# Optimization experiments

Measured on AMD Instinct MI355X. Metric: run time of the kernel, lower is better.

Reference implementation:

```python
import jax, jax.numpy as jnp
import numpy as np

EPS = 1e-5


def setup_inputs() -> dict:
    key = jax.random.key(0)
    ks = jax.random.split(key, 5)
    B, C, H, W = 64, 512, 28, 28
    G = 8
    c_half = C // (2 * G)  # 32
    return {
        "x": jax.random.normal(ks[0], (B, C, H, W), dtype=jnp.float32),
        "cweight": jax.random.normal(ks[1], (c_half,), dtype=jnp.float32),
        "cbias": jax.random.normal(ks[2], (c_half,), dtype=jnp.float32),
        "sweight": jax.random.normal(ks[3], (c_half,), dtype=jnp.float32),
        "sbias": jax.random.normal(ks[4], (c_half,), dtype=jnp.float32),
        "G": G,
    }


def reference(x, cweight, cbias, sweight, sbias, G):
    B, C, H, W = x.shape
    HW = H * W
    Cg = C // G
    c_half = Cg // 2

    # group view: [B*G, Cg, HW]
    xg = x.reshape(B * G, Cg, HW)
    x0 = xg[:, :c_half]   # channel-attention half
    x1 = xg[:, c_half:]   # spatial-attention half

    # channel attention: sigmoid(cweight * avgpool_hw(x0) + cbias), per channel
    m = jnp.mean(x0, axis=-1, keepdims=True)                    # [BG, c_half, 1]
    a0 = jax.nn.sigmoid(cweight[None, :, None] * m + cbias[None, :, None])
    y0 = x0 * a0

    # spatial attention: GN stats over the whole c_half*HW slab per (b,g)
    mu = jnp.mean(x1, axis=(1, 2), keepdims=True)               # [BG, 1, 1]
    var = jnp.mean(x1 * x1, axis=(1, 2), keepdims=True) - mu * mu
    rstd = jax.lax.rsqrt(jnp.maximum(var, 0.0) + EPS)
    norm = (x1 - mu) * rstd
    a1 = jax.nn.sigmoid(sweight[None, :, None] * norm + sbias[None, :, None])
    y1 = x1 * a1

    y = jnp.concatenate([y0, y1], axis=1).reshape(B, C, HW)

    # channel shuffle with 2 groups: out[:, 2*w + g2] = y[:, g2*(C//2) + w]
    y = y.reshape(B, 2, C // 2, HW).transpose(0, 2, 1, 3).reshape(B, C, H, W)
    return y
```

## Files before the change

### kernel.cpp

```cpp
#include <hip/hip_runtime.h>

typedef float f32x4 __attribute__((ext_vector_type(4)));

#define EPSV 1e-5f

__device__ __forceinline__ float sigmoidf_(float z) {
    return 1.0f / (1.0f + __expf(-z));
}

__global__ __launch_bounds__(1024, 4) void fused_sgate_onepass(
    const f32x4* __restrict__ x4,
    const float* __restrict__ cweight,
    const float* __restrict__ cbias,
    const float* __restrict__ sweight,
    const float* __restrict__ sbias,
    f32x4* __restrict__ out4,
    int nX1)
{
    const int tid = threadIdx.x;

    if ((int)blockIdx.x < nX1) {
        const int bg = blockIdx.x;
        const int b  = bg >> 3, g = bg & 7;
        const f32x4* __restrict__ xs = x4 + (size_t)bg * 12544 + 6272;

        f32x4 w[6];
#pragma unroll
        for (int k = 0; k < 6; ++k) w[k] = xs[tid + 1024 * k];
        const bool x1e = (tid < 128);
        f32x4 we = {0.f, 0.f, 0.f, 0.f};
        if (x1e) we = xs[6144 + tid];

        float s = 0.f, ss = 0.f;
#pragma unroll
        for (int k = 0; k < 6; ++k) {
            s  += (w[k].x + w[k].y) + (w[k].z + w[k].w);
            ss += (w[k].x * w[k].x + w[k].y * w[k].y)
                + (w[k].z * w[k].z + w[k].w * w[k].w);
        }
        s  += (we.x + we.y) + (we.z + we.w);
        ss += (we.x * we.x + we.y * we.y) + (we.z * we.z + we.w * we.w);

#pragma unroll
        for (int m = 32; m >= 1; m >>= 1) {
            s  += __shfl_xor(s,  m, 64);
            ss += __shfl_xor(ss, m, 64);
        }

        __shared__ float lds_s[16], lds_ss[16];
        __shared__ float ldsA[32], ldsB[32];
        if ((tid & 63) == 0) { lds_s[tid >> 6] = s; lds_ss[tid >> 6] = ss; }
        __syncthreads();

        if (tid < 32) {
            float S = 0.f, SS = 0.f;
#pragma unroll
            for (int i = 0; i < 16; ++i) { S += lds_s[i]; SS += lds_ss[i]; }
            constexpr float inv_n = 1.0f / (32.0f * 784.0f);
            const float mu   = S * inv_n;
            const float var  = SS * inv_n - mu * mu;
            const float rstd = rsqrtf(fmaxf(var, 0.f) + EPSV);
            const float A    = sweight[tid] * rstd;
            ldsA[tid] = A;
            ldsB[tid] = sbias[tid] - A * mu;
        }
        __syncthreads();

#pragma unroll
        for (int k = 0; k < 6; ++k)
            asm volatile("" : "+v"(w[k].x), "+v"(w[k].y),
                              "+v"(w[k].z), "+v"(w[k].w));

        f32x4* __restrict__ ob = out4 + (size_t)b * 100352;
#pragma unroll
        for (int k = 0; k < 6; ++k) {
            const int idx = tid + 1024 * k;
            const int c1  = idx / 196;
            const int p   = idx - c1 * 196;
            const float A = ldsA[c1], Bq = ldsB[c1];
            f32x4 t = w[k], r;
            r.x = t.x * sigmoidf_(A * t.x + Bq);
            r.y = t.y * sigmoidf_(A * t.y + Bq);
            r.z = t.z * sigmoidf_(A * t.z + Bq);
            r.w = t.w * sigmoidf_(A * t.w + Bq);
            const int c  = g * 64 + 32 + c1;
            const int cp = (c < 256) ? (2 * c) : (2 * (c - 256) + 1);
            __builtin_nontemporal_store(r, ob + (size_t)cp * 196 + p);
        }
        if (x1e) {
            const int idx = 6144 + tid;
            const int c1  = idx / 196;
            const int p   = idx - c1 * 196;
            const float A = ldsA[c1], Bq = ldsB[c1];
            f32x4 t = we, r;
            r.x = t.x * sigmoidf_(A * t.x + Bq);
            r.y = t.y * sigmoidf_(A * t.y + Bq);
            r.z = t.z * sigmoidf_(A * t.z + Bq);
            r.w = t.w * sigmoidf_(A * t.w + Bq);
            const int c  = g * 64 + 32 + c1;
            const int cp = (c < 256) ? (2 * c) : (2 * (c - 256) + 1);
            __builtin_nontemporal_store(r, ob + (size_t)cp * 196 + p);
        }
    } else {
        const int chw = ((int)blockIdx.x - nX1) * 16 + (tid >> 6);
        const int ln  = tid & 63;
        const int bg  = chw >> 5;
        const int cc  = chw & 31;

        const f32x4* __restrict__ xch = x4 + (size_t)bg * 12544 + cc * 196;
        f32x4 v0 = xch[ln];
        f32x4 v1 = xch[64 + ln];
        f32x4 v2 = xch[128 + ln];
        const bool extra = (ln < 4);
        f32x4 v3 = {0.f, 0.f, 0.f, 0.f};
        if (extra) v3 = xch[192 + ln];

        float s = (v0.x + v0.y) + (v0.z + v0.w)
                + (v1.x + v1.y) + (v1.z + v1.w)
                + (v2.x + v2.y) + (v2.z + v2.w)
                + (v3.x + v3.y) + (v3.z + v3.w);
#pragma unroll
        for (int m = 32; m >= 1; m >>= 1) s += __shfl_xor(s, m, 64);

        const float a0 = sigmoidf_(cweight[cc] * (s * (1.0f / 784.0f)) + cbias[cc]);

        const int b = bg >> 3, g = bg & 7;
        const int c  = g * 64 + cc;
        const int cp = (c < 256) ? (2 * c) : (2 * (c - 256) + 1);
        f32x4* __restrict__ och = out4 + (size_t)b * 100352 + (size_t)cp * 196;

        __builtin_nontemporal_store(v0 * a0, &och[ln]);
        __builtin_nontemporal_store(v1 * a0, &och[64 + ln]);
        __builtin_nontemporal_store(v2 * a0, &och[128 + ln]);
        if (extra) __builtin_nontemporal_store(v3 * a0, &och[192 + ln]);
    }
}

extern "C" void kernel_launch(void* const* d_in, const int* in_sizes, int n_in,
                              void* d_out, int out_size, void* d_ws, size_t ws_size,
                              hipStream_t stream) {
    const float* x  = (const float*)d_in[0];
    const float* cw = (const float*)d_in[1];
    const float* cb = (const float*)d_in[2];
    const float* sw = (const float*)d_in[3];
    const float* sb = (const float*)d_in[4];
    float* out = (float*)d_out;

    const int B   = in_sizes[0] / (512 * 784);
    const int nX1 = B * 8;
    const int nX0 = B * 16;

    fused_sgate_onepass<<<nX1 + nX0, 1024, 0, stream>>>(
        (const f32x4*)x, cw, cb, sw, sb, (f32x4*)out, nX1);
}
```

Baseline: 193.9 us.

## Interleave spatial and channel blocks, halve block size, reload x1 slab instead of caching

```diff
diff --git a/kernel.cpp b/kernel.cpp
--- a/kernel.cpp
+++ b/kernel.cpp
@@ -8,38 +8,35 @@
     return 1.0f / (1.0f + __expf(-z));
 }
 
-__global__ __launch_bounds__(1024, 4) void fused_sgate_onepass(
+__global__ __launch_bounds__(512, 8) void fused_sgate_mix(
     const f32x4* __restrict__ x4,
     const float* __restrict__ cweight,
     const float* __restrict__ cbias,
     const float* __restrict__ sweight,
     const float* __restrict__ sbias,
-    f32x4* __restrict__ out4,
-    int nX1)
+    f32x4* __restrict__ out4)
 {
+    const int bid = (int)blockIdx.x;
     const int tid = threadIdx.x;
 
-    if ((int)blockIdx.x < nX1) {
-        const int bg = blockIdx.x;
+    if (bid % 5 == 0) {
+        const int bg = bid / 5;
         const int b  = bg >> 3, g = bg & 7;
         const f32x4* __restrict__ xs = x4 + (size_t)bg * 12544 + 6272;
 
-        f32x4 w[6];
-#pragma unroll
-        for (int k = 0; k < 6; ++k) w[k] = xs[tid + 1024 * k];
-        const bool x1e = (tid < 128);
-        f32x4 we = {0.f, 0.f, 0.f, 0.f};
-        if (x1e) we = xs[6144 + tid];
-
         float s = 0.f, ss = 0.f;
 #pragma unroll
-        for (int k = 0; k < 6; ++k) {
-            s  += (w[k].x + w[k].y) + (w[k].z + w[k].w);
-            ss += (w[k].x * w[k].x + w[k].y * w[k].y)
-                + (w[k].z * w[k].z + w[k].w * w[k].w);
+        for (int k = 0; k < 12; ++k) {
+            f32x4 v = xs[tid + 512 * k];
+            s  += (v.x + v.y) + (v.z + v.w);
+            ss += (v.x * v.x + v.y * v.y) + (v.z * v.z + v.w * v.w);
         }
-        s  += (we.x + we.y) + (we.z + we.w);
-        ss += (we.x * we.x + we.y * we.y) + (we.z * we.z + we.w * we.w);
+        const bool x1e = (tid < 128);
+        if (x1e) {
+            f32x4 v = xs[6144 + tid];
+            s  += (v.x + v.y) + (v.z + v.w);
+            ss += (v.x * v.x + v.y * v.y) + (v.z * v.z + v.w * v.w);
+        }
 
 #pragma unroll
         for (int m = 32; m >= 1; m >>= 1) {
@@ -47,7 +44,7 @@
             ss += __shfl_xor(ss, m, 64);
         }
 
-        __shared__ float lds_s[16], lds_ss[16];
+        __shared__ float lds_s[8], lds_ss[8];
         __shared__ float ldsA[32], ldsB[32];
         if ((tid & 63) == 0) { lds_s[tid >> 6] = s; lds_ss[tid >> 6] = ss; }
         __syncthreads();
@@ -55,7 +52,7 @@
         if (tid < 32) {
             float S = 0.f, SS = 0.f;
 #pragma unroll
-            for (int i = 0; i < 16; ++i) { S += lds_s[i]; SS += lds_ss[i]; }
+            for (int i = 0; i < 8; ++i) { S += lds_s[i]; SS += lds_ss[i]; }
             constexpr float inv_n = 1.0f / (32.0f * 784.0f);
             const float mu   = S * inv_n;
             const float var  = SS * inv_n - mu * mu;
@@ -66,19 +63,14 @@
         }
         __syncthreads();
 
-#pragma unroll
-        for (int k = 0; k < 6; ++k)
-            asm volatile("" : "+v"(w[k].x), "+v"(w[k].y),
-                              "+v"(w[k].z), "+v"(w[k].w));
-
         f32x4* __restrict__ ob = out4 + (size_t)b * 100352;
 #pragma unroll
-        for (int k = 0; k < 6; ++k) {
-            const int idx = tid + 1024 * k;
+        for (int k = 0; k < 12; ++k) {
+            const int idx = tid + 512 * k;
             const int c1  = idx / 196;
             const int p   = idx - c1 * 196;
             const float A = ldsA[c1], Bq = ldsB[c1];
-            f32x4 t = w[k], r;
+            f32x4 t = xs[idx], r;
             r.x = t.x * sigmoidf_(A * t.x + Bq);
             r.y = t.y * sigmoidf_(A * t.y + Bq);
             r.z = t.z * sigmoidf_(A * t.z + Bq);
@@ -92,7 +84,7 @@
             const int c1  = idx / 196;
             const int p   = idx - c1 * 196;
             const float A = ldsA[c1], Bq = ldsB[c1];
-            f32x4 t = we, r;
+            f32x4 t = xs[idx], r;
             r.x = t.x * sigmoidf_(A * t.x + Bq);
             r.y = t.y * sigmoidf_(A * t.y + Bq);
             r.z = t.z * sigmoidf_(A * t.z + Bq);
@@ -102,10 +94,11 @@
             __builtin_nontemporal_store(r, ob + (size_t)cp * 196 + p);
         }
     } else {
-        const int chw = ((int)blockIdx.x - nX1) * 16 + (tid >> 6);
-        const int ln  = tid & 63;
-        const int bg  = chw >> 5;
-        const int cc  = chw & 31;
+        const int x0id = bid - bid / 5 - 1;
+        const int chw  = x0id * 8 + (tid >> 6);
+        const int ln   = tid & 63;
+        const int bg   = chw >> 5;
+        const int cc   = chw & 31;
 
         const f32x4* __restrict__ xch = x4 + (size_t)bg * 12544 + cc * 196;
         f32x4 v0 = xch[ln];
@@ -148,8 +141,8 @@
 
     const int B   = in_sizes[0] / (512 * 784);
     const int nX1 = B * 8;
-    const int nX0 = B * 16;
+    const int nX0 = B * 32;
 
-    fused_sgate_onepass<<<nX1 + nX0, 1024, 0, stream>>>(
-        (const f32x4*)x, cw, cb, sw, sb, (f32x4*)out, nX1);
+    fused_sgate_mix<<<nX1 + nX0, 512, 0, stream>>>(
+        (const f32x4*)x, cw, cb, sw, sb, (f32x4*)out);
 }
```

Result: slower. 219.5 us (+13.2%).

## Stage spatial-half slab in LDS to cut registers and double occupancy

Applied to the files above, without the earlier changes.

```diff
diff --git a/kernel.cpp b/kernel.cpp
--- a/kernel.cpp
+++ b/kernel.cpp
@@ -8,7 +8,7 @@
     return 1.0f / (1.0f + __expf(-z));
 }
 
-__global__ __launch_bounds__(1024, 4) void fused_sgate_onepass(
+__global__ __launch_bounds__(1024, 8) void fused_sgate_lds(
     const f32x4* __restrict__ x4,
     const float* __restrict__ cweight,
     const float* __restrict__ cbias,
@@ -24,31 +24,40 @@
         const int b  = bg >> 3, g = bg & 7;
         const f32x4* __restrict__ xs = x4 + (size_t)bg * 12544 + 6272;
 
-        f32x4 w[6];
-#pragma unroll
-        for (int k = 0; k < 6; ++k) w[k] = xs[tid + 1024 * k];
+        __shared__ f32x4 slab[4096];
+        __shared__ float lds_s[16], lds_ss[16];
+        __shared__ float ldsA[32], ldsB[32];
+
+        f32x4 t0 = xs[tid];
+        f32x4 t1 = xs[1024 + tid];
+        f32x4 t2 = xs[2048 + tid];
+        f32x4 t3 = xs[3072 + tid];
+        f32x4 w0 = xs[4096 + tid];
+        f32x4 w1 = xs[5120 + tid];
         const bool x1e = (tid < 128);
         f32x4 we = {0.f, 0.f, 0.f, 0.f};
         if (x1e) we = xs[6144 + tid];
 
-        float s = 0.f, ss = 0.f;
-#pragma unroll
-        for (int k = 0; k < 6; ++k) {
-            s  += (w[k].x + w[k].y) + (w[k].z + w[k].w);
-            ss += (w[k].x * w[k].x + w[k].y * w[k].y)
-                + (w[k].z * w[k].z + w[k].w * w[k].w);
+        slab[tid]        = t0;
+        slab[1024 + tid] = t1;
+        slab[2048 + tid] = t2;
+        slab[3072 + tid] = t3;
+
+        float s, ss;
+        {
+            f32x4 a = t0 + t1, c = t2 + t3, d = w0 + w1;
+            f32x4 q = t0 * t0 + t1 * t1 + t2 * t2 + t3 * t3
+                    + w0 * w0 + w1 * w1 + we * we;
+            f32x4 sv = a + c + d + we;
+            s  = (sv.x + sv.y) + (sv.z + sv.w);
+            ss = (q.x + q.y) + (q.z + q.w);
         }
-        s  += (we.x + we.y) + (we.z + we.w);
-        ss += (we.x * we.x + we.y * we.y) + (we.z * we.z + we.w * we.w);
 
 #pragma unroll
         for (int m = 32; m >= 1; m >>= 1) {
             s  += __shfl_xor(s,  m, 64);
             ss += __shfl_xor(ss, m, 64);
         }
-
-        __shared__ float lds_s[16], lds_ss[16];
-        __shared__ float ldsA[32], ldsB[32];
         if ((tid & 63) == 0) { lds_s[tid >> 6] = s; lds_ss[tid >> 6] = ss; }
         __syncthreads();
 
@@ -66,40 +75,66 @@
         }
         __syncthreads();
 
-#pragma unroll
-        for (int k = 0; k < 6; ++k)
-            asm volatile("" : "+v"(w[k].x), "+v"(w[k].y),
-                              "+v"(w[k].z), "+v"(w[k].w));
+        asm volatile("" : "+v"(w0.x), "+v"(w0.y), "+v"(w0.z), "+v"(w0.w),
+                          "+v"(w1.x), "+v"(w1.y), "+v"(w1.z), "+v"(w1.w));
 
         f32x4* __restrict__ ob = out4 + (size_t)b * 100352;
 #pragma unroll
-        for (int k = 0; k < 6; ++k) {
+        for (int k = 0; k < 4; ++k) {
             const int idx = tid + 1024 * k;
             const int c1  = idx / 196;
             const int p   = idx - c1 * 196;
             const float A = ldsA[c1], Bq = ldsB[c1];
-            f32x4 t = w[k], r;
-            r.x = t.x * sigmoidf_(A * t.x + Bq);
-            r.y = t.y * sigmoidf_(A * t.y + Bq);
-            r.z = t.z * sigmoidf_(A * t.z + Bq);
-            r.w = t.w * sigmoidf_(A * t.w + Bq);
+            f32x4 v = slab[idx], r;
+            r.x = v.x * sigmoidf_(A * v.x + Bq);
+            r.y = v.y * sigmoidf_(A * v.y + Bq);
+            r.z = v.z * sigmoidf_(A * v.z + Bq);
+            r.w = v.w * sigmoidf_(A * v.w + Bq);
             const int c  = g * 64 + 32 + c1;
             const int cp = (c < 256) ? (2 * c) : (2 * (c - 256) + 1);
-            __builtin_nontemporal_store(r, ob + (size_t)cp * 196 + p);
+            ob[(size_t)cp * 196 + p] = r;
+        }
+        {
+            const int idx = 4096 + tid;
+            const int c1  = idx / 196;
+            const int p   = idx - c1 * 196;
+            const float A = ldsA[c1], Bq = ldsB[c1];
+            f32x4 r;
+            r.x = w0.x * sigmoidf_(A * w0.x + Bq);
+            r.y = w0.y * sigmoidf_(A * w0.y + Bq);
+            r.z = w0.z * sigmoidf_(A * w0.z + Bq);
+            r.w = w0.w * sigmoidf_(A * w0.w + Bq);
+            const int c  = g * 64 + 32 + c1;
+            const int cp = (c < 256) ? (2 * c) : (2 * (c - 256) + 1);
+            ob[(size_t)cp * 196 + p] = r;
+        }
+        {
+            const int idx = 5120 + tid;
+            const int c1  = idx / 196;
+            const int p   = idx - c1 * 196;
+            const float A = ldsA[c1], Bq = ldsB[c1];
+            f32x4 r;
+            r.x = w1.x * sigmoidf_(A * w1.x + Bq);
+            r.y = w1.y * sigmoidf_(A * w1.y + Bq);
+            r.z = w1.z * sigmoidf_(A * w1.z + Bq);
+            r.w = w1.w * sigmoidf_(A * w1.w + Bq);
+            const int c  = g * 64 + 32 + c1;
+            const int cp = (c < 256) ? (2 * c) : (2 * (c - 256) + 1);
+            ob[(size_t)cp * 196 + p] = r;
         }
         if (x1e) {
             const int idx = 6144 + tid;
             const int c1  = idx / 196;
             const int p   = idx - c1 * 196;
             const float A = ldsA[c1], Bq = ldsB[c1];
-            f32x4 t = we, r;
-            r.x = t.x * sigmoidf_(A * t.x + Bq);
-            r.y = t.y * sigmoidf_(A * t.y + Bq);
-            r.z = t.z * sigmoidf_(A * t.z + Bq);
-            r.w = t.w * sigmoidf_(A * t.w + Bq);
+            f32x4 r;
+            r.x = we.x * sigmoidf_(A * we.x + Bq);
+            r.y = we.y * sigmoidf_(A * we.y + Bq);
+            r.z = we.z * sigmoidf_(A * we.z + Bq);
+            r.w = we.w * sigmoidf_(A * we.w + Bq);
             const int c  = g * 64 + 32 + c1;
             const int cp = (c < 256) ? (2 * c) : (2 * (c - 256) + 1);
-            __builtin_nontemporal_store(r, ob + (size_t)cp * 196 + p);
+            ob[(size_t)cp * 196 + p] = r;
         }
     } else {
         const int chw = ((int)blockIdx.x - nX1) * 16 + (tid >> 6);
@@ -129,10 +164,10 @@
         const int cp = (c < 256) ? (2 * c) : (2 * (c - 256) + 1);
         f32x4* __restrict__ och = out4 + (size_t)b * 100352 + (size_t)cp * 196;
 
-        __builtin_nontemporal_store(v0 * a0, &och[ln]);
-        __builtin_nontemporal_store(v1 * a0, &och[64 + ln]);
-        __builtin_nontemporal_store(v2 * a0, &och[128 + ln]);
-        if (extra) __builtin_nontemporal_store(v3 * a0, &och[192 + ln]);
+        och[ln]       = v0 * a0;
+        och[64 + ln]  = v1 * a0;
+        och[128 + ln] = v2 * a0;
+        if (extra) och[192 + ln] = v3 * a0;
     }
 }
 
@@ -150,6 +185,6 @@
     const int nX1 = B * 8;
     const int nX0 = B * 16;
 
-    fused_sgate_onepass<<<nX1 + nX0, 1024, 0, stream>>>(
+    fused_sgate_lds<<<nX1 + nX0, 1024, 0, stream>>>(
         (const f32x4*)x, cw, cb, sw, sb, (f32x4*)out, nX1);
 }
```

Result: no change. 191.7 us (-1.1%).
